# Kernel tuning notes

Hardware: AMD Instinct MI355X
Metric: run time of the kernel (lower is better)

Reference implementation:

```python
import jax, jax.numpy as jnp
import numpy as np

NPOINT = 1024
RADII = (0.1, 0.2)
NSAMPLES = (16, 32)
IN_CH = 64
OUT = 256
EPS = 1e-5


def fps(pts, npoint):
    # pts: (N,3) -> (npoint,) int32 farthest-point-sampling indices (starts at index 0)
    N = pts.shape[0]
    def body(carry, _):
        dists, last = carry
        d = jnp.sum((pts - pts[last]) ** 2, axis=-1)
        dists = jnp.minimum(dists, d)
        nxt = jnp.argmax(dists).astype(jnp.int32)
        return (dists, nxt), last
    _, idx = jax.lax.scan(body, (jnp.full((N,), 1e10, pts.dtype), jnp.int32(0)), None, length=npoint)
    return idx


def ball_query(radius, k, xyz, new_xyz):
    # xyz (B,N,3), new_xyz (B,S,3) -> (B,S,k) int32; first k points within radius,
    # padded with the first in-range index (matches pointnet2 ball_query semantics;
    # each centroid is itself a point so at least one index is always in range).
    N = xyz.shape[1]
    d2 = jnp.sum((new_xyz[:, :, None, :] - xyz[:, None, :, :]) ** 2, axis=-1)  # (B,S,N)
    mask = d2 < radius * radius
    key = jnp.where(mask, jnp.arange(N, dtype=jnp.int32)[None, None, :], N)
    order = jnp.argsort(key, axis=-1)[..., :k]            # (B,S,k)
    sel_key = jnp.take_along_axis(key, order, axis=-1)
    valid = sel_key < N
    first = order[..., :1]
    return jnp.where(valid, order, first).astype(jnp.int32)


def gather(x, idx):
    # x (B,N,C), idx (B,...) -> (B,...,C)
    return jax.vmap(lambda f, i: f[i])(x, idx)


def bn_relu(x, gamma, beta):
    # BatchNorm (training-mode batch statistics) over all axes except channel (last), then ReLU
    axes = tuple(range(x.ndim - 1))
    mean = jnp.mean(x, axis=axes, keepdims=True)
    var = jnp.var(x, axis=axes, keepdims=True)
    return jax.nn.relu((x - mean) * jax.lax.rsqrt(var + EPS) * gamma + beta)


def _forward(xyz, feat, branch_params, fuse_params):
    idx_fps = jax.vmap(lambda p: fps(p, NPOINT))(xyz)     # (B,S)
    new_xyz = gather(xyz, idx_fps)                        # (B,S,3)
    outs = []
    for (r, k), (w1, g1, b1, w2, g2, b2) in zip(zip(RADII, NSAMPLES), branch_params):
        idx = ball_query(r, k, xyz, new_xyz)              # (B,S,k)
        rel = gather(xyz, idx) - new_xyz[:, :, None, :]   # (B,S,k,3)
        x = jnp.concatenate([rel, gather(feat, idx)], axis=-1)  # (B,S,k,Cin+3)
        x = bn_relu(jnp.einsum('bskc,oc->bsko', x, w1), g1, b1)
        x = bn_relu(jnp.einsum('bskc,oc->bsko', x, w2), g2, b2)
        outs.append(jnp.max(x, axis=2))                   # max-pool over nsample -> (B,S,OUT)
    x = jnp.concatenate(outs, axis=-1)                    # (B,S,len(RADII)*OUT)
    wf1, gf1, bf1, wf2, gf2, bf2 = fuse_params
    x = bn_relu(jnp.einsum('bsc,oc->bso', x, wf1), gf1, bf1)
    x = bn_relu(jnp.einsum('bsc,oc->bso', x, wf2), gf2, bf2)
    return new_xyz, x


def setup_inputs():
    key = jax.random.key(0)
    ks = jax.random.split(key, 16)
    B, N = 8, 4096
    xyz = jax.random.uniform(ks[0], (B, N, 3), dtype=jnp.float32)
    feat = jax.random.normal(ks[1], (B, N, IN_CH), dtype=jnp.float32)
    cin, mid = IN_CH + 3, OUT // 2
    def w(k, o, c):
        return jax.random.normal(k, (o, c), dtype=jnp.float32) * np.float32(1.0 / np.sqrt(c))
    inp = {"xyz": xyz, "feat": feat}
    i = 2
    for s in range(len(RADII)):
        inp[f"w1_{s}"] = w(ks[i], mid, cin); i += 1
        inp[f"g1_{s}"] = jnp.ones((mid,), jnp.float32)
        inp[f"b1_{s}"] = jnp.zeros((mid,), jnp.float32)
        inp[f"w2_{s}"] = w(ks[i], OUT, mid); i += 1
        inp[f"g2_{s}"] = jnp.ones((OUT,), jnp.float32)
        inp[f"b2_{s}"] = jnp.zeros((OUT,), jnp.float32)
    inp["wf1"] = w(ks[i], OUT, len(RADII) * OUT); i += 1
    inp["gf1"] = jnp.ones((OUT,), jnp.float32)
    inp["bf1"] = jnp.zeros((OUT,), jnp.float32)
    inp["wf2"] = w(ks[i], OUT, OUT)
    inp["gf2"] = jnp.ones((OUT,), jnp.float32)
    inp["bf2"] = jnp.zeros((OUT,), jnp.float32)
    return inp


def reference(xyz, feat, w1_0, g1_0, b1_0, w2_0, g2_0, b2_0,
              w1_1, g1_1, b1_1, w2_1, g2_1, b2_1,
              wf1, gf1, bf1, wf2, gf2, bf2):
    branch_params = [(w1_0, g1_0, b1_0, w2_0, g2_0, b2_0),
                     (w1_1, g1_1, b1_1, w2_1, g2_1, b2_1)]
    fuse_params = (wf1, gf1, bf1, wf2, gf2, bf2)
    return _forward(xyz, feat, branch_params, fuse_params)
```

## Files before the change

kernel.cpp:

```cpp
#include <hip/hip_runtime.h>


#define DEV __device__ __forceinline__

DEV float d2_nofma(float ax, float ay, float az, float bx, float by, float bz) {
#pragma clang fp contract(off)
  float dx = ax - bx, dy = ay - by, dz = az - bz;
  float s = dx * dx + dy * dy;
  return s + dz * dz;
}

DEV unsigned long long u64max(unsigned long long a, unsigned long long b) {
  return a > b ? a : b;
}

__global__ __launch_bounds__(512) void fps_kernel(
    const float* __restrict__ xyz, int* __restrict__ idx_out,
    float* __restrict__ nx_ws, float* __restrict__ nx_out) {
  __shared__ float sp[4096 * 3];
  __shared__ int hist[1024];
  __shared__ unsigned long long cand[2][8];
  const int b = blockIdx.x, t = threadIdx.x;
  const int w = t >> 6;
  const float* P = xyz + (size_t)b * 12288;
  float px[8], py[8], pz[8], dd[8];
#pragma unroll
  for (int j = 0; j < 8; j++) {
    int pi = t * 8 + j;
    float x = P[pi * 3], y = P[pi * 3 + 1], z = P[pi * 3 + 2];
    px[j] = x; py[j] = y; pz[j] = z; dd[j] = 1e10f;
    sp[pi * 3] = x; sp[pi * 3 + 1] = y; sp[pi * 3 + 2] = z;
  }
  __syncthreads();
  int last = 0;
  for (int it = 0; it < 1024; ++it) {
    if (t == 0) hist[it] = last;
    if (it == 1023) break;
    float lx = sp[last * 3], ly = sp[last * 3 + 1], lz = sp[last * 3 + 2];
#pragma unroll
    for (int j = 0; j < 8; j++) {
      float d = d2_nofma(px[j], py[j], pz[j], lx, ly, lz);
      dd[j] = fminf(dd[j], d);
    }
    float bv = fmaxf(fmaxf(fmaxf(dd[0], dd[1]), fmaxf(dd[2], dd[3])),
                     fmaxf(fmaxf(dd[4], dd[5]), fmaxf(dd[6], dd[7])));
    int bj = 7;
#pragma unroll
    for (int j = 6; j >= 0; j--) bj = (dd[j] == bv) ? j : bj;
    int bi = t * 8 + bj;
    unsigned long long p =
        ((unsigned long long)__float_as_uint(bv) << 32) |
        (unsigned int)(4095 - bi);
#define DPP_MAX_STEP(CTRL)                                                  \
    {                                                                       \
      int lo_ = (int)(unsigned int)(p & 0xffffffffull);                     \
      int hi_ = (int)(unsigned int)(p >> 32);                               \
      int olo_ = __builtin_amdgcn_update_dpp(0, lo_, CTRL, 0xf, 0xf, false);\
      int ohi_ = __builtin_amdgcn_update_dpp(0, hi_, CTRL, 0xf, 0xf, false);\
      unsigned long long q_ =                                               \
          ((unsigned long long)(unsigned int)ohi_ << 32) |                  \
          (unsigned int)olo_;                                               \
      if (q_ > p) p = q_;                                                   \
    }
    DPP_MAX_STEP(0xB1);
    DPP_MAX_STEP(0x4E);
    DPP_MAX_STEP(0x124);
    DPP_MAX_STEP(0x128);
    DPP_MAX_STEP(0x142);
    DPP_MAX_STEP(0x143);
#undef DPP_MAX_STEP
    const int buf = it & 1;
    if ((t & 63) == 63) cand[buf][w] = p;
    __syncthreads();
    unsigned long long c0 = cand[buf][0], c1 = cand[buf][1];
    unsigned long long c2 = cand[buf][2], c3 = cand[buf][3];
    unsigned long long c4 = cand[buf][4], c5 = cand[buf][5];
    unsigned long long c6 = cand[buf][6], c7 = cand[buf][7];
    unsigned long long best =
        u64max(u64max(u64max(c0, c1), u64max(c2, c3)),
               u64max(u64max(c4, c5), u64max(c6, c7)));
    last = 4095 - (int)(unsigned int)(best & 0xffffffffull);
  }
  __syncthreads();
  for (int i = t; i < 1024; i += 512) {
    int id = hist[i];
    idx_out[(size_t)b * 1024 + i] = id;
    float x = sp[id * 3], y = sp[id * 3 + 1], z = sp[id * 3 + 2];
    size_t o = ((size_t)b * 1024 + i) * 3;
    nx_ws[o] = x; nx_ws[o + 1] = y; nx_ws[o + 2] = z;
    nx_out[o] = x; nx_out[o + 1] = y; nx_out[o + 2] = z;
  }
}

__global__ __launch_bounds__(256) void bq_kernel(
    const float* __restrict__ xyz, const float* __restrict__ nx,
    int* __restrict__ out0, int* __restrict__ out1) {
  const int wv = threadIdx.x >> 6, lane = threadIdx.x & 63;
  const int bs = blockIdx.x * 4 + wv;
  const int b = bs >> 10;
  const float* c = nx + (size_t)bs * 3;
  const float cx = c[0], cy = c[1], cz = c[2];
  const float* P = xyz + (size_t)b * 12288;
  const float rr0 = 0.1f * 0.1f, rr1 = 0.2f * 0.2f;
  int c0 = 0, c1 = 0, f0 = -1, f1 = -1;
  const unsigned long long below = (1ull << lane) - 1ull;
  for (int base = 0; base < 4096; base += 64) {
    int p = base + lane;
    float x = P[p * 3], y = P[p * 3 + 1], z = P[p * 3 + 2];
    float d2 = d2_nofma(cx, cy, cz, x, y, z);
    bool in0 = d2 < rr0, in1 = d2 < rr1;
    unsigned long long m0 = __ballot(in0), m1 = __ballot(in1);
    if (in0) {
      int slot = c0 + __popcll(m0 & below);
      if (slot < 16) out0[(size_t)bs * 16 + slot] = p;
    }
    if (in1) {
      int slot = c1 + __popcll(m1 & below);
      if (slot < 32) out1[(size_t)bs * 32 + slot] = p;
    }
    if (f0 < 0 && m0) f0 = base + __ffsll(m0) - 1;
    if (f1 < 0 && m1) f1 = base + __ffsll(m1) - 1;
    c0 += __popcll(m0);
    c1 += __popcll(m1);
    if (c0 >= 16 && c1 >= 32) break;
  }
  if (c0 < 16 && lane >= c0 && lane < 16) out0[(size_t)bs * 16 + lane] = f0;
  if (c1 < 32 && lane >= c1 && lane < 32) out1[(size_t)bs * 32 + lane] = f1;
}

template <int KS>
__global__ __launch_bounds__(256) void g1_kernel(
    const float* __restrict__ xyz, const float* __restrict__ feat,
    const float* __restrict__ nx, const int* __restrict__ idx,
    const float* __restrict__ w1, float* __restrict__ y1,
    float* __restrict__ statp) {
  __shared__ float At[34][132];
  __shared__ float Bt[34][132];
  const int t = threadIdx.x;
  const int g0 = blockIdx.x * 128;
  const int tx = t & 15, ty = t >> 4;
  const int r = t >> 1, half = t & 1;
  const int g = g0 + r;
  const int bs = g / KS;
  const int b = bs >> 10;
  const int id = idx[g];
  const float* fp = feat + ((size_t)(b * 4096 + id)) * 64;
  float rel0 = 0, rel1 = 0, rel2 = 0;
  if (half == 0) {
    const float* cp = nx + (size_t)bs * 3;
    const float* pp = xyz + ((size_t)(b * 4096 + id)) * 3;
    rel0 = pp[0] - cp[0]; rel1 = pp[1] - cp[1]; rel2 = pp[2] - cp[2];
  }
  float acc[8][8];
#pragma unroll
  for (int i = 0; i < 8; i++)
#pragma unroll
    for (int j = 0; j < 8; j++) acc[i][j] = 0.f;

#pragma unroll
  for (int kc = 0; kc < 2; ++kc) {
    const int kb = kc * 34;
    const int kn = kc ? 33 : 34;
    {
      int c0 = half * 17;
      int cn = half ? (kn - 17) : 17;
      for (int u = 0; u < cn; u++) {
        int cabs = kb + c0 + u;
        float v;
        if (cabs < 3) v = (cabs == 0) ? rel0 : ((cabs == 1) ? rel1 : rel2);
        else v = fp[cabs - 3];
        At[c0 + u][r] = v;
      }
    }
    {
      int o = t >> 1;
      const float* wp = w1 + (size_t)o * 67;
      int c0 = half * 17;
      int cn = half ? (kn - 17) : 17;
      for (int u = 0; u < cn; u++) Bt[c0 + u][o] = wp[kb + c0 + u];
    }
    __syncthreads();
#pragma unroll 4
    for (int k = 0; k < kn; k++) {
      float4 a0 = *(const float4*)&At[k][ty * 4];
      float4 a1 = *(const float4*)&At[k][ty * 4 + 64];
      float4 b0 = *(const float4*)&Bt[k][tx * 4];
      float4 b1 = *(const float4*)&Bt[k][tx * 4 + 64];
      float av[8] = {a0.x, a0.y, a0.z, a0.w, a1.x, a1.y, a1.z, a1.w};
      float bv[8] = {b0.x, b0.y, b0.z, b0.w, b1.x, b1.y, b1.z, b1.w};
#pragma unroll
      for (int i = 0; i < 8; i++)
#pragma unroll
        for (int j = 0; j < 8; j++) acc[i][j] = fmaf(av[i], bv[j], acc[i][j]);
    }
    __syncthreads();
  }
#pragma unroll
  for (int i = 0; i < 8; i++) {
    int R = ty * 4 + (i & 3) + ((i >> 2) << 6);
    float4 s0 = {acc[i][0], acc[i][1], acc[i][2], acc[i][3]};
    float4 s1 = {acc[i][4], acc[i][5], acc[i][6], acc[i][7]};
    *(float4*)&y1[((size_t)(g0 + R)) * 128 + tx * 4] = s0;
    *(float4*)&y1[((size_t)(g0 + R)) * 128 + tx * 4 + 64] = s1;
  }
  float s8[8], q8[8];
#pragma unroll
  for (int j = 0; j < 8; j++) {
    float s = 0, q = 0;
#pragma unroll
    for (int i = 0; i < 8; i++) {
      float v = acc[i][j];
      s += v;
      q = fmaf(v, v, q);
    }
    s += __shfl_xor(s, 16); s += __shfl_xor(s, 32);
    q += __shfl_xor(q, 16); q += __shfl_xor(q, 32);
    s8[j] = s; q8[j] = q;
  }
  float* red = &At[0][0];
  const int wvx = t >> 6;
  if ((t & 63) < 16) {
#pragma unroll
    for (int j = 0; j < 8; j++) {
      int col = tx * 4 + (j & 3) + ((j >> 2) << 6);
      red[wvx * 128 + col] = s8[j];
      red[512 + wvx * 128 + col] = q8[j];
    }
  }
  __syncthreads();
  if (t < 128) {
    float s = red[t] + red[128 + t] + red[256 + t] + red[384 + t];
    float q = red[512 + t] + red[640 + t] + red[768 + t] + red[896 + t];
    statp[(size_t)blockIdx.x * 256 + t] = s;
    statp[(size_t)blockIdx.x * 256 + 128 + t] = q;
  }
}

template <int KS>
__global__ __launch_bounds__(256, 2) void g2_kernel(
    const float* __restrict__ y1, const float* __restrict__ w2,
    const float* __restrict__ a1, const float* __restrict__ b1,
    float* __restrict__ pmin, float* __restrict__ pmax,
    float* __restrict__ statp) {
  __shared__ float At[32][132];
  __shared__ float Bt[32][260];
  const int t = threadIdx.x;
  const int g0 = blockIdx.x * 128;
  const int tx = t & 15, ty = t >> 4;
  float acc[8][16];
#pragma unroll
  for (int i = 0; i < 8; i++)
#pragma unroll
    for (int j = 0; j < 16; j++) acc[i][j] = 0.f;

  const int r = t >> 1, halfA = t & 1;
  const float* arow = y1 + (size_t)(g0 + r) * 128;
  for (int kc = 0; kc < 4; kc++) {
    {
      const int cb = kc * 32 + halfA * 16;
#pragma unroll
      for (int q = 0; q < 4; q++) {
        float4 v = *(const float4*)&arow[cb + q * 4];
        float vv[4] = {v.x, v.y, v.z, v.w};
#pragma unroll
        for (int e = 0; e < 4; e++) {
          int cabs = cb + q * 4 + e;
          float x = fmaxf(fmaf(a1[cabs], vv[e], b1[cabs]), 0.f);
          At[halfA * 16 + q * 4 + e][r] = x;
        }
      }
    }
    {
      const float* wrow = w2 + (size_t)t * 128 + kc * 32;
#pragma unroll
      for (int q = 0; q < 8; q++) {
        float4 w4 = *(const float4*)&wrow[q * 4];
        Bt[q * 4 + 0][t] = w4.x; Bt[q * 4 + 1][t] = w4.y;
        Bt[q * 4 + 2][t] = w4.z; Bt[q * 4 + 3][t] = w4.w;
      }
    }
    __syncthreads();
#pragma unroll 4
    for (int k = 0; k < 32; k++) {
      float4 a0 = *(const float4*)&At[k][ty * 4];
      float4 a1v = *(const float4*)&At[k][ty * 4 + 64];
      float4 b0 = *(const float4*)&Bt[k][tx * 4];
      float4 b1v = *(const float4*)&Bt[k][tx * 4 + 64];
      float4 b2v = *(const float4*)&Bt[k][tx * 4 + 128];
      float4 b3v = *(const float4*)&Bt[k][tx * 4 + 192];
      float av[8] = {a0.x, a0.y, a0.z, a0.w, a1v.x, a1v.y, a1v.z, a1v.w};
      float bv[16] = {b0.x, b0.y, b0.z, b0.w, b1v.x, b1v.y, b1v.z, b1v.w,
                      b2v.x, b2v.y, b2v.z, b2v.w, b3v.x, b3v.y, b3v.z, b3v.w};
#pragma unroll
      for (int i = 0; i < 8; i++)
#pragma unroll
        for (int j = 0; j < 16; j++) acc[i][j] = fmaf(av[i], bv[j], acc[i][j]);
    }
    __syncthreads();
  }

  float* red = &At[0][0];
  const int w = t >> 6;
  const bool wrsel = ((t & 48) == 0);
  const int NS = 128 / KS;

#pragma unroll
  for (int h = 0; h < 2; h++)
#pragma unroll
    for (int j = 0; j < 16; j++) {
      float x = acc[h * 4][j] + acc[h * 4 + 1][j] + acc[h * 4 + 2][j] + acc[h * 4 + 3][j];
      x += __shfl_xor(x, 16);
      x += __shfl_xor(x, 32);
      if (wrsel) red[(((w << 1) | h) << 8) + (tx << 2) + (j & 3) + ((j >> 2) << 6)] = x;
    }
  __syncthreads();
  float psum = 0;
  for (int e = 0; e < 8; e++) psum += red[(e << 8) + t];
  __syncthreads();
#pragma unroll
  for (int h = 0; h < 2; h++)
#pragma unroll
    for (int j = 0; j < 16; j++) {
      float x = acc[h * 4][j] * acc[h * 4][j];
      x = fmaf(acc[h * 4 + 1][j], acc[h * 4 + 1][j], x);
      x = fmaf(acc[h * 4 + 2][j], acc[h * 4 + 2][j], x);
      x = fmaf(acc[h * 4 + 3][j], acc[h * 4 + 3][j], x);
      x += __shfl_xor(x, 16);
      x += __shfl_xor(x, 32);
      if (wrsel) red[(((w << 1) | h) << 8) + (tx << 2) + (j & 3) + ((j >> 2) << 6)] = x;
    }
  __syncthreads();
  float psq = 0;
  for (int e = 0; e < 8; e++) psq += red[(e << 8) + t];
  statp[(size_t)blockIdx.x * 512 + t] = psum;
  statp[(size_t)blockIdx.x * 512 + 256 + t] = psq;
  __syncthreads();
#pragma unroll
  for (int h = 0; h < 2; h++)
#pragma unroll
    for (int j = 0; j < 16; j++) {
      float x = fminf(fminf(acc[h * 4][j], acc[h * 4 + 1][j]),
                      fminf(acc[h * 4 + 2][j], acc[h * 4 + 3][j]));
      x = fminf(x, __shfl_xor(x, 16));
      x = fminf(x, __shfl_xor(x, 32));
      if (wrsel) red[(((w << 1) | h) << 8) + (tx << 2) + (j & 3) + ((j >> 2) << 6)] = x;
    }
  __syncthreads();
  for (int cell = t; cell < NS * 256; cell += 256) {
    int sg = cell >> 8, col = cell & 255;
    float val;
    if (KS == 16) {
      int h = sg >> 2, ww = sg & 3;
      val = red[(((ww << 1) | h) << 8) + col];
    } else {
      int h = sg >> 1, w0 = (sg & 1) << 1;
      val = fminf(red[(((w0 << 1) | h) << 8) + col],
                  red[((((w0 + 1) << 1) | h) << 8) + col]);
    }
    pmin[(size_t)(blockIdx.x * NS + sg) * 256 + col] = val;
  }
  __syncthreads();
#pragma unroll
  for (int h = 0; h < 2; h++)
#pragma unroll
    for (int j = 0; j < 16; j++) {
      float x = fmaxf(fmaxf(acc[h * 4][j], acc[h * 4 + 1][j]),
                      fmaxf(acc[h * 4 + 2][j], acc[h * 4 + 3][j]));
      x = fmaxf(x, __shfl_xor(x, 16));
      x = fmaxf(x, __shfl_xor(x, 32));
      if (wrsel) red[(((w << 1) | h) << 8) + (tx << 2) + (j & 3) + ((j >> 2) << 6)] = x;
    }
  __syncthreads();
  for (int cell = t; cell < NS * 256; cell += 256) {
    int sg = cell >> 8, col = cell & 255;
    float val;
    if (KS == 16) {
      int h = sg >> 2, ww = sg & 3;
      val = red[(((ww << 1) | h) << 8) + col];
    } else {
      int h = sg >> 1, w0 = (sg & 1) << 1;
      val = fmaxf(red[(((w0 << 1) | h) << 8) + col],
                  red[((((w0 + 1) << 1) | h) << 8) + col]);
    }
    pmax[(size_t)(blockIdx.x * NS + sg) * 256 + col] = val;
  }
}

__global__ __launch_bounds__(256) void finalize_affine(
    const float* __restrict__ statp, int nb, float invM,
    const float* __restrict__ gamma, const float* __restrict__ beta,
    float* __restrict__ aout, float* __restrict__ bout, int N) {
  const int c = blockIdx.x;
  const int t = threadIdx.x;
  float s = 0, q = 0;
  for (int i = t; i < nb; i += 256) {
    s += statp[(size_t)i * 2 * N + c];
    q += statp[(size_t)i * 2 * N + N + c];
  }
#pragma unroll
  for (int m = 1; m <= 32; m <<= 1) {
    s += __shfl_xor(s, m);
    q += __shfl_xor(q, m);
  }
  __shared__ float rs[4], rq[4];
  if ((t & 63) == 0) { rs[t >> 6] = s; rq[t >> 6] = q; }
  __syncthreads();
  if (t == 0) {
    s = rs[0] + rs[1] + rs[2] + rs[3];
    q = rq[0] + rq[1] + rq[2] + rq[3];
    float mean = s * invM;
    float var = q * invM - mean * mean;
    float ia = gamma[c] * rsqrtf(var + 1e-5f);
    aout[c] = ia;
    bout[c] = beta[c] - mean * ia;
  }
}

__global__ __launch_bounds__(256) void pool_concat(
    const float* __restrict__ pmin, const float* __restrict__ pmax,
    const float* __restrict__ a2, const float* __restrict__ b2,
    float* __restrict__ cat, int off) {
  int i = blockIdx.x * 256 + threadIdx.x;
  int row = i >> 8, c = i & 255;
  float a = a2[c];
  float v = (a > 0.f) ? pmax[i] : pmin[i];
  cat[(size_t)row * 512 + off + c] = fmaxf(fmaf(a, v, b2[c]), 0.f);
}

template <bool AFF>
__global__ __launch_bounds__(256) void f_kernel(
    const float* __restrict__ A, const float* __restrict__ W,
    const float* __restrict__ ain, const float* __restrict__ bin,
    float* __restrict__ Y, int K, float* __restrict__ statp) {
  __shared__ float At[64][68];
  __shared__ float Bt[64][132];
  const int t = threadIdx.x, tx = t & 15, ty = t >> 4;
  const int g0 = blockIdx.x * 64, cb = blockIdx.y;
  float acc[4][8];
#pragma unroll
  for (int i = 0; i < 4; i++)
#pragma unroll
    for (int j = 0; j < 8; j++) acc[i][j] = 0.f;
  const int rA = t >> 2, qA = t & 3;
  const int oB = t >> 1, hB = t & 1;
  const float* arow = A + (size_t)(g0 + rA) * K + qA * 16;
  const float* wrow = W + (size_t)(cb * 128 + oB) * K + hB * 32;
  for (int kc = 0; kc < K; kc += 64) {
    {
#pragma unroll
      for (int q = 0; q < 4; q++) {
        float4 v = *(const float4*)&arow[kc + q * 4];
        float vv[4] = {v.x, v.y, v.z, v.w};
        if constexpr (AFF) {
          int c = kc + qA * 16 + q * 4;
#pragma unroll
          for (int e = 0; e < 4; e++)
            vv[e] = fmaxf(fmaf(ain[c + e], vv[e], bin[c + e]), 0.f);
        }
#pragma unroll
        for (int e = 0; e < 4; e++) At[qA * 16 + q * 4 + e][rA] = vv[e];
      }
    }
    {
#pragma unroll
      for (int q = 0; q < 8; q++) {
        float4 v = *(const float4*)&wrow[kc + q * 4];
        Bt[hB * 32 + q * 4 + 0][oB] = v.x;
        Bt[hB * 32 + q * 4 + 1][oB] = v.y;
        Bt[hB * 32 + q * 4 + 2][oB] = v.z;
        Bt[hB * 32 + q * 4 + 3][oB] = v.w;
      }
    }
    __syncthreads();
#pragma unroll 8
    for (int k = 0; k < 64; k++) {
      float4 a0 = *(const float4*)&At[k][ty * 4];
      float4 b0 = *(const float4*)&Bt[k][tx * 4];
      float4 b1 = *(const float4*)&Bt[k][tx * 4 + 64];
      float av[4] = {a0.x, a0.y, a0.z, a0.w};
      float bv[8] = {b0.x, b0.y, b0.z, b0.w, b1.x, b1.y, b1.z, b1.w};
#pragma unroll
      for (int i = 0; i < 4; i++)
#pragma unroll
        for (int j = 0; j < 8; j++) acc[i][j] = fmaf(av[i], bv[j], acc[i][j]);
    }
    __syncthreads();
  }
#pragma unroll
  for (int i = 0; i < 4; i++) {
    int R = g0 + ty * 4 + i;
    float4 s0 = {acc[i][0], acc[i][1], acc[i][2], acc[i][3]};
    float4 s1 = {acc[i][4], acc[i][5], acc[i][6], acc[i][7]};
    *(float4*)&Y[(size_t)R * 256 + cb * 128 + tx * 4] = s0;
    *(float4*)&Y[(size_t)R * 256 + cb * 128 + tx * 4 + 64] = s1;
  }
  float s8[8], q8[8];
#pragma unroll
  for (int j = 0; j < 8; j++) {
    float s = 0, q = 0;
#pragma unroll
    for (int i = 0; i < 4; i++) {
      float v = acc[i][j];
      s += v;
      q = fmaf(v, v, q);
    }
    s += __shfl_xor(s, 16); s += __shfl_xor(s, 32);
    q += __shfl_xor(q, 16); q += __shfl_xor(q, 32);
    s8[j] = s; q8[j] = q;
  }
  float* red = &At[0][0];
  const int wvx = t >> 6;
  if ((t & 63) < 16) {
#pragma unroll
    for (int j = 0; j < 8; j++) {
      int col = tx * 4 + (j & 3) + ((j >> 2) << 6);
      red[wvx * 128 + col] = s8[j];
      red[512 + wvx * 128 + col] = q8[j];
    }
  }
  __syncthreads();
  if (t < 128) {
    float s = red[t] + red[128 + t] + red[256 + t] + red[384 + t];
    float q = red[512 + t] + red[640 + t] + red[768 + t] + red[896 + t];
    statp[(size_t)blockIdx.x * 512 + cb * 128 + t] = s;
    statp[(size_t)blockIdx.x * 512 + 256 + cb * 128 + t] = q;
  }
}

__global__ __launch_bounds__(256) void final_write(
    const float* __restrict__ y, const float* __restrict__ a,
    const float* __restrict__ b, float* __restrict__ out) {
  int i = blockIdx.x * 256 + threadIdx.x;
  int c = i & 255;
  out[i] = fmaxf(fmaf(a[c], y[i], b[c]), 0.f);
}

static const size_t OFF_IDXFPS = 0;
static const size_t OFF_NEWXYZ = 8192;
static const size_t OFF_IDX0 = 32768;
static const size_t OFF_IDX1 = 163840;
static const size_t OFF_Y1 = 425984;
static const size_t OFF_PMIN = 33980416;
static const size_t OFF_PMAX = 36077568;
static const size_t OFF_STATP = 38174720;
static const size_t OFF_CONCAT = 39223296;
static const size_t OFF_YF1 = 43417600;
static const size_t OFF_YF2 = 45514752;
static const size_t OFF_AFF = 47611904;

extern "C" void kernel_launch(void* const* d_in, const int* in_sizes, int n_in,
                              void* d_out, int out_size, void* d_ws,
                              size_t ws_size, hipStream_t stream) {
  const float* xyz = (const float*)d_in[0];
  const float* feat = (const float*)d_in[1];
  const float* w1_0 = (const float*)d_in[2];
  const float* g1_0 = (const float*)d_in[3];
  const float* b1_0 = (const float*)d_in[4];
  const float* w2_0 = (const float*)d_in[5];
  const float* g2_0 = (const float*)d_in[6];
  const float* b2_0 = (const float*)d_in[7];
  const float* w1_1 = (const float*)d_in[8];
  const float* g1_1 = (const float*)d_in[9];
  const float* b1_1 = (const float*)d_in[10];
  const float* w2_1 = (const float*)d_in[11];
  const float* g2_1 = (const float*)d_in[12];
  const float* b2_1 = (const float*)d_in[13];
  const float* wf1 = (const float*)d_in[14];
  const float* gf1 = (const float*)d_in[15];
  const float* bf1 = (const float*)d_in[16];
  const float* wf2 = (const float*)d_in[17];
  const float* gf2 = (const float*)d_in[18];
  const float* bf2 = (const float*)d_in[19];

  float* out = (float*)d_out;
  float* ws = (float*)d_ws;

  int* idxfps = (int*)(ws + OFF_IDXFPS);
  float* nx = ws + OFF_NEWXYZ;
  int* idx0 = (int*)(ws + OFF_IDX0);
  int* idx1 = (int*)(ws + OFF_IDX1);
  float* y1 = ws + OFF_Y1;
  float* pmin = ws + OFF_PMIN;
  float* pmax = ws + OFF_PMAX;
  float* statp = ws + OFF_STATP;
  float* cat = ws + OFF_CONCAT;
  float* yf1 = ws + OFF_YF1;
  float* yf2 = ws + OFF_YF2;
  float* a1 = ws + OFF_AFF;
  float* b1 = a1 + 128;
  float* a2 = b1 + 128;
  float* b2 = a2 + 256;
  float* af1 = b2 + 256;
  float* bf1a = af1 + 256;
  float* af2 = bf1a + 256;
  float* bf2a = af2 + 256;

  fps_kernel<<<8, 512, 0, stream>>>(xyz, idxfps, nx, out);
  bq_kernel<<<2048, 256, 0, stream>>>(xyz, nx, idx0, idx1);

  g1_kernel<16><<<1024, 256, 0, stream>>>(xyz, feat, nx, idx0, w1_0, y1, statp);
  finalize_affine<<<128, 256, 0, stream>>>(statp, 1024, 1.f / 131072.f, g1_0, b1_0, a1, b1, 128);
  g2_kernel<16><<<1024, 256, 0, stream>>>(y1, w2_0, a1, b1, pmin, pmax, statp);
  finalize_affine<<<256, 256, 0, stream>>>(statp, 1024, 1.f / 131072.f, g2_0, b2_0, a2, b2, 256);
  pool_concat<<<8192, 256, 0, stream>>>(pmin, pmax, a2, b2, cat, 0);

  g1_kernel<32><<<2048, 256, 0, stream>>>(xyz, feat, nx, idx1, w1_1, y1, statp);
  finalize_affine<<<128, 256, 0, stream>>>(statp, 2048, 1.f / 262144.f, g1_1, b1_1, a1, b1, 128);
  g2_kernel<32><<<2048, 256, 0, stream>>>(y1, w2_1, a1, b1, pmin, pmax, statp);
  finalize_affine<<<256, 256, 0, stream>>>(statp, 2048, 1.f / 262144.f, g2_1, b2_1, a2, b2, 256);
  pool_concat<<<8192, 256, 0, stream>>>(pmin, pmax, a2, b2, cat, 256);

  f_kernel<false><<<dim3(128, 2), 256, 0, stream>>>(cat, wf1, nullptr, nullptr, yf1, 512, statp);
  finalize_affine<<<256, 256, 0, stream>>>(statp, 128, 1.f / 8192.f, gf1, bf1, af1, bf1a, 256);
  f_kernel<true><<<dim3(128, 2), 256, 0, stream>>>(yf1, wf2, af1, bf1a, yf2, 256, statp);
  finalize_affine<<<256, 256, 0, stream>>>(statp, 128, 1.f / 8192.f, gf2, bf2, af2, bf2a, 256);
  final_write<<<8192, 256, 0, stream>>>(yf2, af2, bf2a, out + 24576);
}
```

Before: 1.386 ms.

## Run second branch GEMM on bf16 MFMA with split-precision hi/lo operands

Replaces the fp32 FMA outer-product GEMM in g2_kernel with bf16 MFMA 16x16x32 instructions. Each fp32 operand is split into a bf16 high and low part and three products are accumulated to keep near-fp32 accuracy. Weights are pre-split by a new small kernel into workspace, and activations are split in LDS after the BN+ReLU affine. The statistics and min/max pooling reductions are rewritten to match the MFMA accumulator layout. This trades three MFMAs per tile and some conversion work for much higher matrix throughput, at some risk to numerical accuracy.

```diff
diff --git a/kernel.cpp b/kernel.cpp
--- a/kernel.cpp
+++ b/kernel.cpp
@@ -1,7 +1,11 @@
 #include <hip/hip_runtime.h>
+#include <hip/hip_bf16.h>
 
 
 #define DEV __device__ __forceinline__
+
+typedef __attribute__((ext_vector_type(8))) short short8v;
+typedef __attribute__((ext_vector_type(4))) float float4v;
 
 DEV float d2_nofma(float ax, float ay, float az, float bx, float by, float bz) {
 #pragma clang fp contract(off)
@@ -12,6 +16,14 @@
 
 DEV unsigned long long u64max(unsigned long long a, unsigned long long b) {
   return a > b ? a : b;
+}
+
+DEV void bsplit(float x, short& h, short& l) {
+  __hip_bfloat16 hb = __float2bfloat16(x);
+  float hf = __bfloat162float(hb);
+  __hip_bfloat16 lb = __float2bfloat16(x - hf);
+  h = *reinterpret_cast<short*>(&hb);
+  l = *reinterpret_cast<short*>(&lb);
 }
 
 __global__ __launch_bounds__(512) void fps_kernel(
@@ -126,6 +138,16 @@
   }
   if (c0 < 16 && lane >= c0 && lane < 16) out0[(size_t)bs * 16 + lane] = f0;
   if (c1 < 32 && lane >= c1 && lane < 32) out1[(size_t)bs * 32 + lane] = f1;
+}
+
+__global__ __launch_bounds__(256) void w2split_kernel(
+    const float* __restrict__ w, short* __restrict__ h,
+    short* __restrict__ l) {
+  int i = blockIdx.x * 256 + threadIdx.x;
+  short hb, lb;
+  bsplit(w[i], hb, lb);
+  h[i] = hb;
+  l[i] = lb;
 }
 
 template <int KS>
@@ -238,151 +260,143 @@
 
 template <int KS>
 __global__ __launch_bounds__(256, 2) void g2_kernel(
-    const float* __restrict__ y1, const float* __restrict__ w2,
-    const float* __restrict__ a1, const float* __restrict__ b1,
-    float* __restrict__ pmin, float* __restrict__ pmax,
-    float* __restrict__ statp) {
-  __shared__ float At[32][132];
-  __shared__ float Bt[32][260];
+    const float* __restrict__ y1, const short* __restrict__ w2h,
+    const short* __restrict__ w2l, const float* __restrict__ a1,
+    const float* __restrict__ b1, float* __restrict__ pmin,
+    float* __restrict__ pmax, float* __restrict__ statp) {
+  __shared__ __align__(16) short Abuf[2][128][136];
   const int t = threadIdx.x;
+  const int wv = t >> 6, lane = t & 63;
   const int g0 = blockIdx.x * 128;
-  const int tx = t & 15, ty = t >> 4;
-  float acc[8][16];
-#pragma unroll
-  for (int i = 0; i < 8; i++)
-#pragma unroll
-    for (int j = 0; j < 16; j++) acc[i][j] = 0.f;
-
-  const int r = t >> 1, halfA = t & 1;
-  const float* arow = y1 + (size_t)(g0 + r) * 128;
-  for (int kc = 0; kc < 4; kc++) {
-    {
-      const int cb = kc * 32 + halfA * 16;
-#pragma unroll
-      for (int q = 0; q < 4; q++) {
-        float4 v = *(const float4*)&arow[cb + q * 4];
-        float vv[4] = {v.x, v.y, v.z, v.w};
-#pragma unroll
-        for (int e = 0; e < 4; e++) {
-          int cabs = cb + q * 4 + e;
-          float x = fmaxf(fmaf(a1[cabs], vv[e], b1[cabs]), 0.f);
-          At[halfA * 16 + q * 4 + e][r] = x;
+
+  {
+    const int r = t >> 1, half = t & 1;
+    const float* arow = y1 + (size_t)(g0 + r) * 128 + half * 64;
+#pragma unroll
+    for (int q = 0; q < 8; q++) {
+      float4 v0 = *(const float4*)&arow[q * 8];
+      float4 v1 = *(const float4*)&arow[q * 8 + 4];
+      float vv[8] = {v0.x, v0.y, v0.z, v0.w, v1.x, v1.y, v1.z, v1.w};
+      short8v h8, l8;
+#pragma unroll
+      for (int e = 0; e < 8; e++) {
+        int cabs = half * 64 + q * 8 + e;
+        float x = fmaxf(fmaf(a1[cabs], vv[e], b1[cabs]), 0.f);
+        short hh, ll;
+        bsplit(x, hh, ll);
+        h8[e] = hh; l8[e] = ll;
+      }
+      *(short8v*)&Abuf[0][r][half * 64 + q * 8] = h8;
+      *(short8v*)&Abuf[1][r][half * 64 + q * 8] = l8;
+    }
+  }
+  __syncthreads();
+
+  const int kgo = (lane >> 4) * 8;
+  short8v ahf[2][4], alf[2][4];
+#pragma unroll
+  for (int mt = 0; mt < 2; mt++)
+#pragma unroll
+    for (int kg = 0; kg < 4; kg++) {
+      int rr = wv * 32 + mt * 16 + (lane & 15);
+      ahf[mt][kg] = *(const short8v*)&Abuf[0][rr][kg * 32 + kgo];
+      alf[mt][kg] = *(const short8v*)&Abuf[1][rr][kg * 32 + kgo];
+    }
+  __syncthreads();
+
+  float4v acc[2][16];
+#pragma unroll
+  for (int mt = 0; mt < 2; mt++)
+#pragma unroll
+    for (int nt = 0; nt < 16; nt++) acc[mt][nt] = (float4v){0.f, 0.f, 0.f, 0.f};
+
+#pragma unroll
+  for (int kg = 0; kg < 4; kg++) {
+#pragma unroll
+    for (int nt = 0; nt < 16; nt++) {
+      const int brow = nt * 16 + (lane & 15);
+      const size_t bo = (size_t)brow * 128 + kg * 32 + kgo;
+      short8v bh = *(const short8v*)&w2h[bo];
+      short8v bl = *(const short8v*)&w2l[bo];
+#pragma unroll
+      for (int mt = 0; mt < 2; mt++) {
+        acc[mt][nt] = __builtin_amdgcn_mfma_f32_16x16x32_bf16(
+            ahf[mt][kg], bh, acc[mt][nt], 0, 0, 0);
+        acc[mt][nt] = __builtin_amdgcn_mfma_f32_16x16x32_bf16(
+            alf[mt][kg], bh, acc[mt][nt], 0, 0, 0);
+        acc[mt][nt] = __builtin_amdgcn_mfma_f32_16x16x32_bf16(
+            ahf[mt][kg], bl, acc[mt][nt], 0, 0, 0);
+      }
+    }
+  }
+
+  float* red = (float*)&Abuf[0][0][0];
+#pragma unroll
+  for (int nt = 0; nt < 16; nt++) {
+    float s = 0, q = 0;
+#pragma unroll
+    for (int mt = 0; mt < 2; mt++)
+#pragma unroll
+      for (int j = 0; j < 4; j++) {
+        float v = acc[mt][nt][j];
+        s += v;
+        q = fmaf(v, v, q);
+      }
+    s += __shfl_xor(s, 16); s += __shfl_xor(s, 32);
+    q += __shfl_xor(q, 16); q += __shfl_xor(q, 32);
+    if (lane < 16) {
+      red[wv * 256 + nt * 16 + lane] = s;
+      red[1024 + wv * 256 + nt * 16 + lane] = q;
+    }
+  }
+  __syncthreads();
+  {
+    float s = red[t] + red[256 + t] + red[512 + t] + red[768 + t];
+    float q = red[1024 + t] + red[1280 + t] + red[1536 + t] + red[1792 + t];
+    statp[(size_t)blockIdx.x * 512 + t] = s;
+    statp[(size_t)blockIdx.x * 512 + 256 + t] = q;
+  }
+
+  if (KS == 32) {
+#pragma unroll
+    for (int nt = 0; nt < 16; nt++) {
+      float mn = acc[0][nt][0], mx = acc[0][nt][0];
+#pragma unroll
+      for (int mt = 0; mt < 2; mt++)
+#pragma unroll
+        for (int j = 0; j < 4; j++) {
+          float v = acc[mt][nt][j];
+          mn = fminf(mn, v);
+          mx = fmaxf(mx, v);
         }
-      }
-    }
-    {
-      const float* wrow = w2 + (size_t)t * 128 + kc * 32;
-#pragma unroll
-      for (int q = 0; q < 8; q++) {
-        float4 w4 = *(const float4*)&wrow[q * 4];
-        Bt[q * 4 + 0][t] = w4.x; Bt[q * 4 + 1][t] = w4.y;
-        Bt[q * 4 + 2][t] = w4.z; Bt[q * 4 + 3][t] = w4.w;
-      }
-    }
-    __syncthreads();
-#pragma unroll 4
-    for (int k = 0; k < 32; k++) {
-      float4 a0 = *(const float4*)&At[k][ty * 4];
-      float4 a1v = *(const float4*)&At[k][ty * 4 + 64];
-      float4 b0 = *(const float4*)&Bt[k][tx * 4];
-      float4 b1v = *(const float4*)&Bt[k][tx * 4 + 64];
-      float4 b2v = *(const float4*)&Bt[k][tx * 4 + 128];
-      float4 b3v = *(const float4*)&Bt[k][tx * 4 + 192];
-      float av[8] = {a0.x, a0.y, a0.z, a0.w, a1v.x, a1v.y, a1v.z, a1v.w};
-      float bv[16] = {b0.x, b0.y, b0.z, b0.w, b1v.x, b1v.y, b1v.z, b1v.w,
-                      b2v.x, b2v.y, b2v.z, b2v.w, b3v.x, b3v.y, b3v.z, b3v.w};
-#pragma unroll
-      for (int i = 0; i < 8; i++)
-#pragma unroll
-        for (int j = 0; j < 16; j++) acc[i][j] = fmaf(av[i], bv[j], acc[i][j]);
-    }
-    __syncthreads();
-  }
-
-  float* red = &At[0][0];
-  const int w = t >> 6;
-  const bool wrsel = ((t & 48) == 0);
-  const int NS = 128 / KS;
-
-#pragma unroll
-  for (int h = 0; h < 2; h++)
-#pragma unroll
-    for (int j = 0; j < 16; j++) {
-      float x = acc[h * 4][j] + acc[h * 4 + 1][j] + acc[h * 4 + 2][j] + acc[h * 4 + 3][j];
-      x += __shfl_xor(x, 16);
-      x += __shfl_xor(x, 32);
-      if (wrsel) red[(((w << 1) | h) << 8) + (tx << 2) + (j & 3) + ((j >> 2) << 6)] = x;
-    }
-  __syncthreads();
-  float psum = 0;
-  for (int e = 0; e < 8; e++) psum += red[(e << 8) + t];
-  __syncthreads();
-#pragma unroll
-  for (int h = 0; h < 2; h++)
-#pragma unroll
-    for (int j = 0; j < 16; j++) {
-      float x = acc[h * 4][j] * acc[h * 4][j];
-      x = fmaf(acc[h * 4 + 1][j], acc[h * 4 + 1][j], x);
-      x = fmaf(acc[h * 4 + 2][j], acc[h * 4 + 2][j], x);
-      x = fmaf(acc[h * 4 + 3][j], acc[h * 4 + 3][j], x);
-      x += __shfl_xor(x, 16);
-      x += __shfl_xor(x, 32);
-      if (wrsel) red[(((w << 1) | h) << 8) + (tx << 2) + (j & 3) + ((j >> 2) << 6)] = x;
-    }
-  __syncthreads();
-  float psq = 0;
-  for (int e = 0; e < 8; e++) psq += red[(e << 8) + t];
-  statp[(size_t)blockIdx.x * 512 + t] = psum;
-  statp[(size_t)blockIdx.x * 512 + 256 + t] = psq;
-  __syncthreads();
-#pragma unroll
-  for (int h = 0; h < 2; h++)
-#pragma unroll
-    for (int j = 0; j < 16; j++) {
-      float x = fminf(fminf(acc[h * 4][j], acc[h * 4 + 1][j]),
-                      fminf(acc[h * 4 + 2][j], acc[h * 4 + 3][j]));
-      x = fminf(x, __shfl_xor(x, 16));
-      x = fminf(x, __shfl_xor(x, 32));
-      if (wrsel) red[(((w << 1) | h) << 8) + (tx << 2) + (j & 3) + ((j >> 2) << 6)] = x;
-    }
-  __syncthreads();
-  for (int cell = t; cell < NS * 256; cell += 256) {
-    int sg = cell >> 8, col = cell & 255;
-    float val;
-    if (KS == 16) {
-      int h = sg >> 2, ww = sg & 3;
-      val = red[(((ww << 1) | h) << 8) + col];
-    } else {
-      int h = sg >> 1, w0 = (sg & 1) << 1;
-      val = fminf(red[(((w0 << 1) | h) << 8) + col],
-                  red[((((w0 + 1) << 1) | h) << 8) + col]);
-    }
-    pmin[(size_t)(blockIdx.x * NS + sg) * 256 + col] = val;
-  }
-  __syncthreads();
-#pragma unroll
-  for (int h = 0; h < 2; h++)
-#pragma unroll
-    for (int j = 0; j < 16; j++) {
-      float x = fmaxf(fmaxf(acc[h * 4][j], acc[h * 4 + 1][j]),
-                      fmaxf(acc[h * 4 + 2][j], acc[h * 4 + 3][j]));
-      x = fmaxf(x, __shfl_xor(x, 16));
-      x = fmaxf(x, __shfl_xor(x, 32));
-      if (wrsel) red[(((w << 1) | h) << 8) + (tx << 2) + (j & 3) + ((j >> 2) << 6)] = x;
-    }
-  __syncthreads();
-  for (int cell = t; cell < NS * 256; cell += 256) {
-    int sg = cell >> 8, col = cell & 255;
-    float val;
-    if (KS == 16) {
-      int h = sg >> 2, ww = sg & 3;
-      val = red[(((ww << 1) | h) << 8) + col];
-    } else {
-      int h = sg >> 1, w0 = (sg & 1) << 1;
-      val = fmaxf(red[(((w0 << 1) | h) << 8) + col],
-                  red[((((w0 + 1) << 1) | h) << 8) + col]);
-    }
-    pmax[(size_t)(blockIdx.x * NS + sg) * 256 + col] = val;
+      mn = fminf(mn, __shfl_xor(mn, 16)); mn = fminf(mn, __shfl_xor(mn, 32));
+      mx = fmaxf(mx, __shfl_xor(mx, 16)); mx = fmaxf(mx, __shfl_xor(mx, 32));
+      if (lane < 16) {
+        size_t o = (size_t)(blockIdx.x * 4 + wv) * 256 + nt * 16 + lane;
+        pmin[o] = mn;
+        pmax[o] = mx;
+      }
+    }
+  } else {
+#pragma unroll
+    for (int mt = 0; mt < 2; mt++)
+#pragma unroll
+      for (int nt = 0; nt < 16; nt++) {
+        float mn = acc[mt][nt][0], mx = acc[mt][nt][0];
+#pragma unroll
+        for (int j = 1; j < 4; j++) {
+          float v = acc[mt][nt][j];
+          mn = fminf(mn, v);
+          mx = fmaxf(mx, v);
+        }
+        mn = fminf(mn, __shfl_xor(mn, 16)); mn = fminf(mn, __shfl_xor(mn, 32));
+        mx = fmaxf(mx, __shfl_xor(mx, 16)); mx = fmaxf(mx, __shfl_xor(mx, 32));
+        if (lane < 16) {
+          size_t o = (size_t)(blockIdx.x * 8 + wv * 2 + mt) * 256 + nt * 16 + lane;
+          pmin[o] = mn;
+          pmax[o] = mx;
+        }
+      }
   }
 }
 
@@ -594,19 +608,25 @@
   float* bf1a = af1 + 256;
   float* af2 = bf1a + 256;
   float* bf2a = af2 + 256;
-
+  short* w2h0 = (short*)yf1;
+  short* w2l0 = w2h0 + 32768;
+  short* w2h1 = w2l0 + 32768;
+  short* w2l1 = w2h1 + 32768;
+
+  w2split_kernel<<<128, 256, 0, stream>>>(w2_0, w2h0, w2l0);
+  w2split_kernel<<<128, 256, 0, stream>>>(w2_1, w2h1, w2l1);
   fps_kernel<<<8, 512, 0, stream>>>(xyz, idxfps, nx, out);
   bq_kernel<<<2048, 256, 0, stream>>>(xyz, nx, idx0, idx1);
 
   g1_kernel<16><<<1024, 256, 0, stream>>>(xyz, feat, nx, idx0, w1_0, y1, statp);
   finalize_affine<<<128, 256, 0, stream>>>(statp, 1024, 1.f / 131072.f, g1_0, b1_0, a1, b1, 128);
-  g2_kernel<16><<<1024, 256, 0, stream>>>(y1, w2_0, a1, b1, pmin, pmax, statp);
+  g2_kernel<16><<<1024, 256, 0, stream>>>(y1, w2h0, w2l0, a1, b1, pmin, pmax, statp);
   finalize_affine<<<256, 256, 0, stream>>>(statp, 1024, 1.f / 131072.f, g2_0, b2_0, a2, b2, 256);
   pool_concat<<<8192, 256, 0, stream>>>(pmin, pmax, a2, b2, cat, 0);
 
   g1_kernel<32><<<2048, 256, 0, stream>>>(xyz, feat, nx, idx1, w1_1, y1, statp);
   finalize_affine<<<128, 256, 0, stream>>>(statp, 2048, 1.f / 262144.f, g1_1, b1_1, a1, b1, 128);
-  g2_kernel<32><<<2048, 256, 0, stream>>>(y1, w2_1, a1, b1, pmin, pmax, statp);
+  g2_kernel<32><<<2048, 256, 0, stream>>>(y1, w2h1, w2l1, a1, b1, pmin, pmax, statp);
   finalize_affine<<<256, 256, 0, stream>>>(statp, 2048, 1.f / 262144.f, g2_1, b2_1, a2, b2, 256);
   pool_concat<<<8192, 256, 0, stream>>>(pmin, pmax, a2, b2, cat, 256);
 
```

New measurement: 1.312 ms. 5.3% less time.
